# Performance work log

Hardware: AMD Instinct MI355X
Metric: run time of the kernel (lower is better)

The kernel has to match this reference:

```python
import jax, jax.numpy as jnp
import numpy as np
from jax.scipy.special import logsumexp

B, N, D = 8, 1500, 256
ITERS = 50


def _mlp(x, W1, b1, W2, b2, W3, b3):
    # DETR-style MLP: ReLU between layers, linear last
    h = jax.nn.relu(x @ W1 + b1)
    h = jax.nn.relu(h @ W2 + b2)
    return h @ W3 + b3


def _log_sinkhorn(Z, log_mu, log_nu, iters):
    # Z: [b, m+1, n+1]; loop-carried dual potentials u, v
    u0 = jnp.zeros_like(log_mu)
    v0 = jnp.zeros_like(log_nu)

    def step(carry, _):
        u, v = carry
        u = log_mu - logsumexp(Z + v[:, None, :], axis=2)
        v = log_nu - logsumexp(Z + u[:, :, None], axis=1)
        return (u, v), None

    (u, v), _ = jax.lax.scan(step, (u0, v0), None, length=iters)
    return Z + u[:, :, None] + v[:, None, :]


def _log_optimal_transport(scores, alpha, iters):
    b, m, n = scores.shape
    bins0 = jnp.broadcast_to(alpha, (b, m, 1))
    bins1 = jnp.broadcast_to(alpha, (b, 1, n))
    a = jnp.broadcast_to(alpha, (b, 1, 1))
    couplings = jnp.concatenate(
        [jnp.concatenate([scores, bins0], -1), jnp.concatenate([bins1, a], -1)], 1
    )  # [b, m+1, n+1]
    dt = scores.dtype
    norm = -jnp.log(jnp.asarray(m + n, dt))
    log_mu = jnp.concatenate([jnp.full((m,), norm, dt), jnp.log(jnp.asarray(n, dt))[None] + norm])
    log_nu = jnp.concatenate([jnp.full((n,), norm, dt), jnp.log(jnp.asarray(m, dt))[None] + norm])
    log_mu = jnp.broadcast_to(log_mu[None], (b, m + 1))
    log_nu = jnp.broadcast_to(log_nu[None], (b, n + 1))
    Z = _log_sinkhorn(couplings, log_mu, log_nu, iters)
    return Z - norm


def setup_inputs() -> dict:
    key = jax.random.key(0)
    k = jax.random.split(key, 6)
    s = 0.05
    return {
        "quer_feat": jax.random.normal(k[0], (B, N, D), jnp.float32),
        "pos_start": jax.random.normal(k[1], (B, N, D), jnp.float32),
        "pos_end": jax.random.normal(k[2], (B, N, D), jnp.float32),
        "W1": jax.random.normal(k[3], (2 * D, D), jnp.float32) * s,
        "b1": jnp.zeros((D,), jnp.float32),
        "W2": jax.random.normal(k[4], (D, D), jnp.float32) * s,
        "b2": jnp.zeros((D,), jnp.float32),
        "W3": jax.random.normal(k[5], (D, D), jnp.float32) * s,
        "b3": jnp.zeros((D,), jnp.float32),
        "bin_score": jnp.asarray(1.0, jnp.float32),
        "iters": ITERS,
    }


def reference(quer_feat, pos_start, pos_end, W1, b1, W2, b2, W3, b3, bin_score, iters):
    # forward_single with shared_projection + similarity_based + sinkhorn
    f1 = _mlp(jnp.concatenate([quer_feat, pos_end], -1), W1, b1, W2, b2, W3, b3)
    f2 = _mlp(jnp.concatenate([quer_feat, pos_start], -1), W1, b1, W2, b2, W3, b3)
    scores = jnp.einsum("bnc,bmc->bnm", f1, f2) / jnp.sqrt(jnp.asarray(D, f1.dtype))
    i = jnp.arange(scores.shape[1])
    scores = scores.at[:, i, i].set(-jnp.inf)  # no self-connection
    Z = _log_optimal_transport(scores, bin_score, iters)
    return jnp.exp(Z)
```

## Files before the change

### kernel.cpp

```cpp
#include <hip/hip_runtime.h>
#include <hip/hip_fp16.h>

#define BATCH 8
#define NPTS 1500
#define DIM 256
#define M1 1501
#define KH 1536
#define MROWS 24000
#define ITERS 50
#define MU_PT (1.0f / 3000.0f)
#define MU_BIN 0.5f

typedef _Float16 half8 __attribute__((ext_vector_type(8)));
typedef float f32x4 __attribute__((ext_vector_type(4)));

__device__ __forceinline__ float4 ld4(const float* p){ return *(const float4*)p; }

__global__ void prep_w_kernel(const float* __restrict__ W1, const float* __restrict__ W2,
                              const float* __restrict__ W3, __half* __restrict__ Wt1,
                              __half* __restrict__ Wt2, __half* __restrict__ Wt3)
{
  int gid = blockIdx.x * 256 + threadIdx.x;
  if (gid < 512 * 256) {
    int n = gid >> 9, k = gid & 511;
    Wt1[gid] = __float2half(W1[k * 256 + n]);
  } else if (gid < 512 * 256 + 256 * 256) {
    int g = gid - 512 * 256; int n = g >> 8, k = g & 255;
    Wt2[g] = __float2half(W2[k * 256 + n]);
  } else if (gid < 512 * 256 + 2 * 256 * 256) {
    int g = gid - 512 * 256 - 256 * 256; int n = g >> 8, k = g & 255;
    Wt3[g] = __float2half(W3[k * 256 + n]);
  }
}

template<int MODE>
__global__ __launch_bounds__(256) void mfma_gemm_kernel(
    const float* __restrict__ Aq, const float* __restrict__ Ap_end,
    const float* __restrict__ Ap_start, const __half* __restrict__ Ah,
    const __half* __restrict__ Bh, const float* __restrict__ bias,
    __half* __restrict__ out)
{
  const int K = (MODE == 0) ? 512 : 256;
  const int M = (MODE == 3) ? NPTS : MROWS;
  __shared__ _Float16 As[128][40];
  __shared__ _Float16 Bs[128][40];
  const int t = threadIdx.x;
  const int lane = t & 63;
  const int wave = t >> 6;
  const int quad = lane >> 4, l15 = lane & 15;
  const int wm = wave & 1, wn = wave >> 1;
  const int m0 = blockIdx.x * 128;
  const int n0 = blockIdx.y * 128;
  const int b  = (MODE == 3) ? blockIdx.z : 0;
  const __half* F1 = Ah + (size_t)b * NPTS * 256;
  const __half* F2 = Ah + (size_t)(12000 + b * NPTS) * 256;

  f32x4 acc[4][4];
#pragma unroll
  for (int i = 0; i < 4; ++i)
#pragma unroll
    for (int j = 0; j < 4; ++j) acc[i][j] = (f32x4){0.f, 0.f, 0.f, 0.f};

  const int sr = t >> 1;
  const int c0 = (t & 1) * 16;

  for (int kt = 0; kt < K; kt += 32) {
    {
      int grow = m0 + sr;
      if (MODE == 0) {
        union { half8 v[2]; _Float16 s[16]; } U;
        if (grow < M) {
          int col = kt + c0;
          int r12 = (grow < 12000) ? grow : grow - 12000;
          const float* src;
          if (col < 256) src = Aq + (size_t)r12 * 256 + col;
          else src = ((grow < 12000) ? Ap_end : Ap_start) + (size_t)r12 * 256 + (col - 256);
#pragma unroll
          for (int i = 0; i < 4; ++i) {
            float4 w = ld4(src + 4 * i);
            U.s[4*i+0] = (_Float16)w.x; U.s[4*i+1] = (_Float16)w.y;
            U.s[4*i+2] = (_Float16)w.z; U.s[4*i+3] = (_Float16)w.w;
          }
        } else {
#pragma unroll
          for (int i = 0; i < 16; ++i) U.s[i] = (_Float16)0.f;
        }
        *(half8*)&As[sr][c0]     = U.v[0];
        *(half8*)&As[sr][c0 + 8] = U.v[1];
      } else {
        const __half* src = ((MODE == 3) ? F1 : Ah) + (size_t)grow * 256 + kt + c0;
        uint4 u0 = make_uint4(0,0,0,0), u1 = make_uint4(0,0,0,0);
        if (grow < M) { u0 = *(const uint4*)src; u1 = *(const uint4*)(src + 8); }
        *(uint4*)&As[sr][c0]     = u0;
        *(uint4*)&As[sr][c0 + 8] = u1;
      }
    }
    {
      int n = n0 + sr;
      uint4 u0 = make_uint4(0,0,0,0), u1 = make_uint4(0,0,0,0);
      if (MODE == 3) {
        if (n < NPTS) {
          const __half* src = F2 + (size_t)n * 256 + kt + c0;
          u0 = *(const uint4*)src; u1 = *(const uint4*)(src + 8);
        }
      } else {
        const __half* src = Bh + (size_t)n * K + kt + c0;
        u0 = *(const uint4*)src; u1 = *(const uint4*)(src + 8);
      }
      *(uint4*)&Bs[sr][c0]     = u0;
      *(uint4*)&Bs[sr][c0 + 8] = u1;
    }
    __syncthreads();
    half8 af[4], bf[4];
#pragma unroll
    for (int sm = 0; sm < 4; ++sm)
      af[sm] = *(half8*)&As[wm * 64 + sm * 16 + l15][quad * 8];
#pragma unroll
    for (int sn = 0; sn < 4; ++sn)
      bf[sn] = *(half8*)&Bs[wn * 64 + sn * 16 + l15][quad * 8];
#pragma unroll
    for (int sm = 0; sm < 4; ++sm)
#pragma unroll
      for (int sn = 0; sn < 4; ++sn)
        acc[sm][sn] = __builtin_amdgcn_mfma_f32_16x16x32_f16(af[sm], bf[sn], acc[sm][sn], 0, 0, 0);
    __syncthreads();
  }

  if (MODE == 3) {
    __half* Kb = out + (size_t)b * M1 * KH;
#pragma unroll
    for (int sm = 0; sm < 4; ++sm) {
      int rbase = m0 + wm * 64 + sm * 16 + quad * 4;
#pragma unroll
      for (int reg = 0; reg < 4; ++reg) {
        int gi = rbase + reg;
        if (gi < NPTS) {
#pragma unroll
          for (int sn = 0; sn < 4; ++sn) {
            int gj = n0 + wn * 64 + sn * 16 + l15;
            float v = acc[sm][sn][reg] * 0.0625f;
            float kv = (gj < NPTS && gj != gi) ? __expf(v) : 0.f;
            Kb[(size_t)gi * KH + gj] = __float2half(kv);
          }
        }
      }
    }
  } else {
    float bv[4];
#pragma unroll
    for (int sn = 0; sn < 4; ++sn) bv[sn] = bias[n0 + wn * 64 + sn * 16 + l15];
#pragma unroll
    for (int sm = 0; sm < 4; ++sm) {
      int rbase = m0 + wm * 64 + sm * 16 + quad * 4;
#pragma unroll
      for (int reg = 0; reg < 4; ++reg) {
        int gr = rbase + reg;
        if (gr < MROWS) {
#pragma unroll
          for (int sn = 0; sn < 4; ++sn) {
            int col = n0 + wn * 64 + sn * 16 + l15;
            float v = acc[sm][sn][reg] + bv[sn];
            if (MODE != 2) v = fmaxf(v, 0.f);
            out[(size_t)gr * 256 + col] = __float2half(v);
          }
        }
      }
    }
  }
}

__global__ void bins_kernel(__half* __restrict__ Kh, const float* __restrict__ palpha,
                            float* __restrict__ csum0)
{
  int gid = blockIdx.x * 256 + threadIdx.x;
  if (gid >= BATCH * KH) return;
  int b = gid / KH, x = gid % KH;
  __half He = __float2half(expf(palpha[0]));
  __half* Kb = Kh + (size_t)b * M1 * KH;
  csum0[gid] = 0.f;
  if (x < M1) {
    Kb[(size_t)NPTS * KH + x] = He;
    Kb[(size_t)x * KH + NPTS] = He;
  } else {
    Kb[(size_t)NPTS * KH + x] = __float2half(0.f);
  }
}

__global__ __launch_bounds__(256) void sink_iter_kernel(
    const __half* __restrict__ Kh,
    const float* __restrict__ csum_prev,
    float* __restrict__ csum_cur,
    float* __restrict__ csum_zero,
    float* __restrict__ eu, int first, int wr_eu)
{
  const int t = threadIdx.x;
  const int wave = t >> 6, lane = t & 63;
  const int bb = blockIdx.x & 7;
  const int rb = blockIdx.x >> 3;
  const int wv = (rb << 2) | wave;
  const __half* Kb = Kh + (size_t)bb * M1 * KH;
  float* eub = eu + bb * KH;

  __shared__ __align__(16) float wpart[4][KH];

  if (rb == 0) {
    for (int j = t; j < KH; j += 256) csum_zero[bb * KH + j] = 0.f;
  }

  float ev[24];
  if (first) {
#pragma unroll
    for (int k = 0; k < 3; ++k) {
      int cbase = (lane << 3) + (k << 9);
#pragma unroll
      for (int j = 0; j < 8; ++j) ev[k * 8 + j] = (cbase + j < M1) ? 1.0f : 0.f;
    }
  } else {
    const float* cp = csum_prev + bb * KH;
#pragma unroll
    for (int k = 0; k < 3; ++k) {
      int cbase = (lane << 3) + (k << 9);
      float4 a  = *(const float4*)(cp + cbase);
      float4 bq = *(const float4*)(cp + cbase + 4);
      float cs[8] = {a.x, a.y, a.z, a.w, bq.x, bq.y, bq.z, bq.w};
#pragma unroll
      for (int j = 0; j < 8; ++j) {
        int col = cbase + j;
        float nu = (col < NPTS) ? MU_PT : ((col == NPTS) ? MU_BIN : 0.f);
        ev[k * 8 + j] = (col < M1) ? (nu / cs[j]) : 0.f;
      }
    }
  }

  float acc[24];
#pragma unroll
  for (int k = 0; k < 24; ++k) acc[k] = 0.f;

  for (int i = wv; i < M1; i += 1024) {
    const int iB = i + 512;
    const bool hasB = (iB < M1);
    const __half* rowA = Kb + (size_t)i * KH;
    const __half* rowB = Kb + (size_t)(hasB ? iB : i) * KH;

    uint4 ua[3], ub[3];
#pragma unroll
    for (int k = 0; k < 3; ++k) ua[k] = *(const uint4*)(rowA + ((lane + (k << 6)) << 3));
#pragma unroll
    for (int k = 0; k < 3; ++k) ub[k] = *(const uint4*)(rowB + ((lane + (k << 6)) << 3));

    {
      float r[24], dot = 0.f;
#pragma unroll
      for (int k = 0; k < 3; ++k) {
        union { uint4 u; __half2 h[4]; } U; U.u = ua[k];
#pragma unroll
        for (int m = 0; m < 4; ++m) {
          float2 f = __half22float2(U.h[m]);
          r[k * 8 + 2 * m]     = f.x;
          r[k * 8 + 2 * m + 1] = f.y;
        }
        dot += r[k*8+0]*ev[k*8+0] + r[k*8+1]*ev[k*8+1] + r[k*8+2]*ev[k*8+2] + r[k*8+3]*ev[k*8+3]
             + r[k*8+4]*ev[k*8+4] + r[k*8+5]*ev[k*8+5] + r[k*8+6]*ev[k*8+6] + r[k*8+7]*ev[k*8+7];
      }
#pragma unroll
      for (int off = 32; off > 0; off >>= 1) dot += __shfl_xor(dot, off);
      float mu = (i < NPTS) ? MU_PT : MU_BIN;
      float euv = mu / dot;
      if (wr_eu && lane == 0) eub[i] = euv;
#pragma unroll
      for (int k = 0; k < 24; ++k) acc[k] += r[k] * euv;
    }
    if (hasB) {
      float r[24], dot = 0.f;
#pragma unroll
      for (int k = 0; k < 3; ++k) {
        union { uint4 u; __half2 h[4]; } U; U.u = ub[k];
#pragma unroll
        for (int m = 0; m < 4; ++m) {
          float2 f = __half22float2(U.h[m]);
          r[k * 8 + 2 * m]     = f.x;
          r[k * 8 + 2 * m + 1] = f.y;
        }
        dot += r[k*8+0]*ev[k*8+0] + r[k*8+1]*ev[k*8+1] + r[k*8+2]*ev[k*8+2] + r[k*8+3]*ev[k*8+3]
             + r[k*8+4]*ev[k*8+4] + r[k*8+5]*ev[k*8+5] + r[k*8+6]*ev[k*8+6] + r[k*8+7]*ev[k*8+7];
      }
#pragma unroll
      for (int off = 32; off > 0; off >>= 1) dot += __shfl_xor(dot, off);
      float mu = (iB < NPTS) ? MU_PT : MU_BIN;
      float euv = mu / dot;
      if (wr_eu && lane == 0) eub[iB] = euv;
#pragma unroll
      for (int k = 0; k < 24; ++k) acc[k] += r[k] * euv;
    }
  }

#pragma unroll
  for (int k = 0; k < 3; ++k) {
    int c = lane + (k << 6);
    float4 a0 = make_float4(acc[k*8+0], acc[k*8+1], acc[k*8+2], acc[k*8+3]);
    float4 a1 = make_float4(acc[k*8+4], acc[k*8+5], acc[k*8+6], acc[k*8+7]);
    *(float4*)&wpart[wave][(c << 3)]     = a0;
    *(float4*)&wpart[wave][(c << 3) + 4] = a1;
  }
  __syncthreads();
  for (int j = t; j < M1; j += 256) {
    float s = wpart[0][j] + wpart[1][j] + wpart[2][j] + wpart[3][j];
    atomicAdd(&csum_cur[bb * KH + j], s);
  }
}

__global__ void final_ev_kernel(const float* __restrict__ csum,
                                float* __restrict__ ev)
{
  int j = blockIdx.x * 256 + threadIdx.x;
  int bb = blockIdx.y;
  if (j >= M1) return;
  float nu = (j < NPTS) ? MU_PT : MU_BIN;
  ev[bb * KH + j] = nu / csum[bb * KH + j];
}

__global__ __launch_bounds__(256) void finalize_kernel(
    const __half* __restrict__ Kh, const float* __restrict__ eu,
    const float* __restrict__ ev, float* __restrict__ out)
{
  int rowid = blockIdx.x * 4 + (threadIdx.x >> 6);
  if (rowid >= BATCH * M1) return;
  int lane = threadIdx.x & 63;
  int b = rowid / M1, i = rowid % M1;
  const __half* krow = Kh + ((size_t)b * M1 + i) * KH;
  const float* evb = ev + b * KH;
  float* orow = out + (size_t)rowid * M1;
  float scale = eu[b * KH + i] * 3000.0f;
#pragma unroll
  for (int k = 0; k < 24; ++k) {
    int c = lane + (k << 6);
    if (c < M1)
      orow[c] = __half2float(krow[c]) * evb[c] * scale;
  }
}

extern "C" void kernel_launch(void* const* d_in, const int* in_sizes, int n_in,
                              void* d_out, int out_size, void* d_ws, size_t ws_size,
                              hipStream_t stream)
{
  const float* quer      = (const float*)d_in[0];
  const float* pos_start = (const float*)d_in[1];
  const float* pos_end   = (const float*)d_in[2];
  const float* W1 = (const float*)d_in[3];
  const float* b1 = (const float*)d_in[4];
  const float* W2 = (const float*)d_in[5];
  const float* b2 = (const float*)d_in[6];
  const float* W3 = (const float*)d_in[7];
  const float* b3 = (const float*)d_in[8];
  const float* alpha = (const float*)d_in[9];

  char* ws = (char*)d_ws;
  size_t off = 0;
  auto carve = [&](size_t bytes) -> void* {
    void* p = ws + off;
    off += (bytes + 1023) & ~(size_t)1023;
    return p;
  };
  __half* Ha  = (__half*)carve((size_t)MROWS * 256 * 2);
  __half* Hb  = (__half*)carve((size_t)MROWS * 256 * 2);
  __half* Kh  = (__half*)carve((size_t)BATCH * M1 * KH * 2);
  __half* Wt1 = (__half*)carve((size_t)256 * 512 * 2);
  __half* Wt2 = (__half*)carve((size_t)256 * 256 * 2);
  __half* Wt3 = (__half*)carve((size_t)256 * 256 * 2);
  float* csum[3];
  for (int c = 0; c < 3; ++c) csum[c] = (float*)carve((size_t)BATCH * KH * 4);
  float* eu = (float*)carve((size_t)BATCH * KH * 4);
  float* ev = (float*)carve((size_t)BATCH * KH * 4);
  (void)ws_size; (void)in_sizes; (void)n_in; (void)out_size;

  dim3 blk(256);
  prep_w_kernel<<<dim3(1024), blk, 0, stream>>>(W1, W2, W3, Wt1, Wt2, Wt3);
  mfma_gemm_kernel<0><<<dim3(188, 2), blk, 0, stream>>>(quer, pos_end, pos_start, nullptr, Wt1, b1, Ha);
  mfma_gemm_kernel<1><<<dim3(188, 2), blk, 0, stream>>>(nullptr, nullptr, nullptr, Ha, Wt2, b2, Hb);
  mfma_gemm_kernel<2><<<dim3(188, 2), blk, 0, stream>>>(nullptr, nullptr, nullptr, Hb, Wt3, b3, Ha);
  mfma_gemm_kernel<3><<<dim3(12, 12, 8), blk, 0, stream>>>(nullptr, nullptr, nullptr, Ha, nullptr, nullptr, Kh);
  bins_kernel<<<dim3((BATCH * KH + 255) / 256), blk, 0, stream>>>(Kh, alpha, csum[0]);
  for (int it = 0; it < ITERS; ++it) {
    float* prev = csum[(it + 2) % 3];
    float* cur  = csum[it % 3];
    float* znxt = csum[(it + 1) % 3];
    sink_iter_kernel<<<dim3(1024), blk, 0, stream>>>(Kh, prev, cur, znxt, eu,
                                                     it == 0 ? 1 : 0,
                                                     it == ITERS - 1 ? 1 : 0);
  }
  final_ev_kernel<<<dim3(6, 8), blk, 0, stream>>>(csum[(ITERS - 1) % 3], ev);
  finalize_kernel<<<dim3((BATCH * M1 + 3) / 4), blk, 0, stream>>>(Kh, eu, ev, (float*)d_out);
}
```

Measured before the change: 798.0 us.

## Give each Sinkhorn wave six rows with all loads issued up front, halving the grid

The Sinkhorn iteration kernel now runs with half as many blocks. Each wave handles six fixed rows spaced 256 apart instead of looping over pairs of rows. All 18 vector loads per lane are issued before any compute, to raise memory-level parallelism and halve the per-column atomic adds into the column sums. The last two rows use nontemporal loads, which could reduce cache retention of the kernel matrix that is re-read on every iteration. The extra live registers may also lower occupancy.

```diff
diff --git a/kernel.cpp b/kernel.cpp
--- a/kernel.cpp
+++ b/kernel.cpp
@@ -13,6 +13,7 @@
 
 typedef _Float16 half8 __attribute__((ext_vector_type(8)));
 typedef float f32x4 __attribute__((ext_vector_type(4)));
+typedef unsigned int u32x4 __attribute__((ext_vector_type(4)));
 
 __device__ __forceinline__ float4 ld4(const float* p){ return *(const float4*)p; }
 
@@ -186,6 +187,31 @@
   }
 }
 
+#define PROCESS_ROW(UARR, I)                                                  \
+  {                                                                           \
+    float r[24], dot = 0.f;                                                   \
+    _Pragma("unroll")                                                         \
+    for (int k = 0; k < 3; ++k) {                                             \
+      union { u32x4 u; __half2 h[4]; } U; U.u = UARR[k];                      \
+      _Pragma("unroll")                                                       \
+      for (int m = 0; m < 4; ++m) {                                           \
+        float2 f = __half22float2(U.h[m]);                                    \
+        r[k * 8 + 2 * m]     = f.x;                                           \
+        r[k * 8 + 2 * m + 1] = f.y;                                           \
+      }                                                                       \
+      dot += r[k*8+0]*ev[k*8+0] + r[k*8+1]*ev[k*8+1] + r[k*8+2]*ev[k*8+2]     \
+           + r[k*8+3]*ev[k*8+3] + r[k*8+4]*ev[k*8+4] + r[k*8+5]*ev[k*8+5]     \
+           + r[k*8+6]*ev[k*8+6] + r[k*8+7]*ev[k*8+7];                         \
+    }                                                                         \
+    _Pragma("unroll")                                                         \
+    for (int off = 32; off > 0; off >>= 1) dot += __shfl_xor(dot, off);       \
+    float mu = ((I) < NPTS) ? MU_PT : MU_BIN;                                 \
+    float euv = mu / dot;                                                     \
+    if (wr_eu && lane == 0) eub[(I)] = euv;                                   \
+    _Pragma("unroll")                                                         \
+    for (int k = 0; k < 24; ++k) acc[k] += r[k] * euv;                        \
+  }
+
 __global__ __launch_bounds__(256) void sink_iter_kernel(
     const __half* __restrict__ Kh,
     const float* __restrict__ csum_prev,
@@ -236,62 +262,37 @@
 #pragma unroll
   for (int k = 0; k < 24; ++k) acc[k] = 0.f;
 
-  for (int i = wv; i < M1; i += 1024) {
-    const int iB = i + 512;
-    const bool hasB = (iB < M1);
-    const __half* rowA = Kb + (size_t)i * KH;
-    const __half* rowB = Kb + (size_t)(hasB ? iB : i) * KH;
-
-    uint4 ua[3], ub[3];
-#pragma unroll
-    for (int k = 0; k < 3; ++k) ua[k] = *(const uint4*)(rowA + ((lane + (k << 6)) << 3));
-#pragma unroll
-    for (int k = 0; k < 3; ++k) ub[k] = *(const uint4*)(rowB + ((lane + (k << 6)) << 3));
-
-    {
-      float r[24], dot = 0.f;
-#pragma unroll
-      for (int k = 0; k < 3; ++k) {
-        union { uint4 u; __half2 h[4]; } U; U.u = ua[k];
-#pragma unroll
-        for (int m = 0; m < 4; ++m) {
-          float2 f = __half22float2(U.h[m]);
-          r[k * 8 + 2 * m]     = f.x;
-          r[k * 8 + 2 * m + 1] = f.y;
-        }
-        dot += r[k*8+0]*ev[k*8+0] + r[k*8+1]*ev[k*8+1] + r[k*8+2]*ev[k*8+2] + r[k*8+3]*ev[k*8+3]
-             + r[k*8+4]*ev[k*8+4] + r[k*8+5]*ev[k*8+5] + r[k*8+6]*ev[k*8+6] + r[k*8+7]*ev[k*8+7];
-      }
-#pragma unroll
-      for (int off = 32; off > 0; off >>= 1) dot += __shfl_xor(dot, off);
-      float mu = (i < NPTS) ? MU_PT : MU_BIN;
-      float euv = mu / dot;
-      if (wr_eu && lane == 0) eub[i] = euv;
-#pragma unroll
-      for (int k = 0; k < 24; ++k) acc[k] += r[k] * euv;
-    }
-    if (hasB) {
-      float r[24], dot = 0.f;
-#pragma unroll
-      for (int k = 0; k < 3; ++k) {
-        union { uint4 u; __half2 h[4]; } U; U.u = ub[k];
-#pragma unroll
-        for (int m = 0; m < 4; ++m) {
-          float2 f = __half22float2(U.h[m]);
-          r[k * 8 + 2 * m]     = f.x;
-          r[k * 8 + 2 * m + 1] = f.y;
-        }
-        dot += r[k*8+0]*ev[k*8+0] + r[k*8+1]*ev[k*8+1] + r[k*8+2]*ev[k*8+2] + r[k*8+3]*ev[k*8+3]
-             + r[k*8+4]*ev[k*8+4] + r[k*8+5]*ev[k*8+5] + r[k*8+6]*ev[k*8+6] + r[k*8+7]*ev[k*8+7];
-      }
-#pragma unroll
-      for (int off = 32; off > 0; off >>= 1) dot += __shfl_xor(dot, off);
-      float mu = (iB < NPTS) ? MU_PT : MU_BIN;
-      float euv = mu / dot;
-      if (wr_eu && lane == 0) eub[iB] = euv;
-#pragma unroll
-      for (int k = 0; k < 24; ++k) acc[k] += r[k] * euv;
-    }
+  {
+    const int i0 = wv,        i0b = wv + 256;
+    const int i1 = wv + 512,  i1b = wv + 768;
+    const int i2 = wv + 1024, i2b = wv + 1280;
+    const bool has2b = (i2b < M1);
+
+    const __half* p0a = Kb + (size_t)i0  * KH;
+    const __half* p0b = Kb + (size_t)i0b * KH;
+    const __half* p1a = Kb + (size_t)i1  * KH;
+    const __half* p1b = Kb + (size_t)i1b * KH;
+    const __half* p2a = Kb + (size_t)i2  * KH;
+    const __half* p2b = Kb + (size_t)(has2b ? i2b : i2) * KH;
+
+    u32x4 A0[3], B0[3], A1[3], B1[3], A2[3], B2[3];
+#pragma unroll
+    for (int k = 0; k < 3; ++k) {
+      const int o = (lane + (k << 6)) << 3;
+      A0[k] = *(const u32x4*)(p0a + o);
+      B0[k] = *(const u32x4*)(p0b + o);
+      A1[k] = *(const u32x4*)(p1a + o);
+      B1[k] = *(const u32x4*)(p1b + o);
+      A2[k] = __builtin_nontemporal_load((const u32x4*)(p2a + o));
+      B2[k] = __builtin_nontemporal_load((const u32x4*)(p2b + o));
+    }
+
+    PROCESS_ROW(A0, i0)
+    PROCESS_ROW(B0, i0b)
+    PROCESS_ROW(A1, i1)
+    PROCESS_ROW(B1, i1b)
+    PROCESS_ROW(A2, i2)
+    if (has2b) PROCESS_ROW(B2, i2b)
   }
 
 #pragma unroll
@@ -384,9 +385,9 @@
     float* prev = csum[(it + 2) % 3];
     float* cur  = csum[it % 3];
     float* znxt = csum[(it + 1) % 3];
-    sink_iter_kernel<<<dim3(1024), blk, 0, stream>>>(Kh, prev, cur, znxt, eu,
-                                                     it == 0 ? 1 : 0,
-                                                     it == ITERS - 1 ? 1 : 0);
+    sink_iter_kernel<<<dim3(512), blk, 0, stream>>>(Kh, prev, cur, znxt, eu,
+                                                    it == 0 ? 1 : 0,
+                                                    it == ITERS - 1 ? 1 : 0);
   }
   final_ev_kernel<<<dim3(6, 8), blk, 0, stream>>>(csum[(ITERS - 1) % 3], ev);
   finalize_kernel<<<dim3((BATCH * M1 + 3) / 4), blk, 0, stream>>>(Kh, eu, ev, (float*)d_out);
```

New measurement: 646.2 us. -19.0%, faster.
